# Optimization experiments

Hardware: AMD Instinct MI355X
Metric: run time of the kernel (lower is better)

Reference implementation:

```python
import jax, jax.numpy as jnp
import numpy as np

D_BRICK = 512  # args.brick_vector_dimension
H = 512        # hidden width


def setup_inputs() -> dict:
    key = jax.random.key(0)
    ks = jax.random.split(key, 20)
    B, N = 4, 192

    def w(k, shape, fan_in):
        return jax.random.uniform(k, shape, jnp.float32, -1.0, 1.0) / np.sqrt(fan_in)

    return {
        "brick_vectors": jax.random.normal(ks[0], (B, N, D_BRICK), jnp.float32),
        "xy": jax.random.uniform(ks[1], (B, N, 2), jnp.float32),
        # linear_xy: 2 -> 512
        "W_xy": w(ks[2], (H, 2), 2), "b_xy": w(ks[3], (H,), 2),
        # linear_a: D -> 512
        "W_a": w(ks[4], (H, D_BRICK), D_BRICK), "b_a": w(ks[5], (H,), D_BRICK),
        # linear_b: 512 -> 512
        "W_b": w(ks[6], (H, H), H), "b_b": w(ks[7], (H,), H),
        # combination_a: 1024 -> 512
        "W_ca": w(ks[8], (H, 2 * H), 2 * H), "b_ca": w(ks[9], (H,), 2 * H),
        # combination_b: 512 -> 512
        "W_cb": w(ks[10], (H, H), H), "b_cb": w(ks[11], (H,), H),
        # combination_c: 512 -> 512
        "W_cc": w(ks[12], (H, H), H), "b_cc": w(ks[13], (H,), H),
        # edge_out: 512 -> 2
        "W_out": w(ks[14], (2, H), H), "b_out": w(ks[15], (2,), H),
    }


def reference(brick_vectors, xy, W_xy, b_xy, W_a, b_a, W_b, b_b,
              W_ca, b_ca, W_cb, b_cb, W_cc, b_cc, W_out, b_out):
    # per-brick feature MLP: (B, N, 512)
    f = jnp.einsum('bnd,hd->bnh', brick_vectors, W_a) + b_a \
        + jnp.einsum('bnt,ht->bnh', xy, W_xy) + b_xy
    f = jax.nn.relu(f)
    f = jax.nn.relu(jnp.einsum('bnh,gh->bng', f, W_b) + b_b)

    # combination_a on concat(f[b,j], f[b,i]) without materializing the
    # (B, N, N, 1024) tensor: split the weight into the two 512 halves.
    # edge[b,i,j] = cat(features_a, features_b) where features_a = f[b,j]
    # (expanded over dim 1) and features_b = f[b,i] (expanded over dim 2).
    W1, W2 = W_ca[:, :H], W_ca[:, H:]
    u = jnp.einsum('bnh,gh->bng', f, W1)  # contribution from f[b, j]
    v = jnp.einsum('bnh,gh->bng', f, W2)  # contribution from f[b, i]
    e = jax.nn.relu(u[:, None, :, :] + v[:, :, None, :] + b_ca)  # (B,N,N,512)

    e = jax.nn.relu(jnp.einsum('bijh,gh->bijg', e, W_cb) + b_cb)
    e = jax.nn.relu(jnp.einsum('bijh,gh->bijg', e, W_cc) + b_cc)
    return jnp.einsum('bijh,oh->bijo', e, W_out) + b_out  # (B, N, N, 2)
```

## Files before the change

kernel.cpp:

```cpp
#include <hip/hip_runtime.h>


typedef short  short8  __attribute__((ext_vector_type(8)));
typedef short  short4v __attribute__((ext_vector_type(4)));
typedef float  f32x4   __attribute__((ext_vector_type(4)));

#define LDSW 520

__device__ inline unsigned short f2bf(float x) {
  unsigned u = __float_as_uint(x);
  unsigned r = (u + 0x7FFFu + ((u >> 16) & 1u)) >> 16;
  return (unsigned short)r;
}

__device__ __host__ inline int wtile_off(int c, int k) {
  return ((c >> 4) * 16 + (k >> 5)) * 512 + (c & 15) * 32 + (k & 31);
}

template <int MT, int NT>
__device__ inline void zero_acc(f32x4 (&acc)[MT][NT]) {
#pragma unroll
  for (int mt = 0; mt < MT; ++mt)
#pragma unroll
    for (int nt = 0; nt < NT; ++nt) {
      f32x4 z = {0.f, 0.f, 0.f, 0.f};
      acc[mt][nt] = z;
    }
}

template <int MT, int NT>
__device__ inline void gemm_kloop(const short* E, const short* __restrict__ W,
                                  int lane, int nbase, f32x4 (&acc)[MT][NT]) {
  const int mrow = lane & 15, kg = lane >> 4;
  const short* El = E + mrow * LDSW + kg * 8;
  const short* Wl = W + (nbase >> 4) * 8192 + mrow * 32 + kg * 8;
  short8 wF[2][NT];
#pragma unroll
  for (int nt = 0; nt < NT; ++nt) wF[0][nt] = *(const short8*)(Wl + nt * 8192);
#pragma unroll
  for (int ks = 0; ks < 16; ++ks) {
    const int cur = ks & 1, nxt = cur ^ 1;
    if (ks < 15) {
      const int k1 = (ks + 1) * 512;
#pragma unroll
      for (int nt = 0; nt < NT; ++nt)
        wF[nxt][nt] = *(const short8*)(Wl + nt * 8192 + k1);
    }
    const int k0 = ks * 32;
    short8 e0 = *(const short8*)(El + k0);
#pragma unroll
    for (int mt = 0; mt < MT; ++mt) {
      const short8 ecur = e0;
      if (mt < MT - 1) e0 = *(const short8*)(El + (mt + 1) * 16 * LDSW + k0);
#pragma unroll
      for (int nt = 0; nt < NT; ++nt)
        acc[mt][nt] = __builtin_amdgcn_mfma_f32_16x16x32_bf16(
            wF[cur][nt], ecur, acc[mt][nt], 0, 0, 0);
    }
  }
}

template <int MT, int NT>
__device__ inline void store_relu_lds(short* E, const float* __restrict__ bias,
                                      int lane, int nbase, f32x4 (&acc)[MT][NT]) {
  const int mrow = lane & 15, kg = lane >> 4;
#pragma unroll
  for (int nt = 0; nt < NT; ++nt) {
    const int oc = nbase + nt * 16 + kg * 4;
    const float4 bs = *(const float4*)(bias + oc);
#pragma unroll
    for (int mt = 0; mt < MT; ++mt) {
      short4v s;
      s.x = (short)f2bf(fmaxf(acc[mt][nt][0] + bs.x, 0.f));
      s.y = (short)f2bf(fmaxf(acc[mt][nt][1] + bs.y, 0.f));
      s.z = (short)f2bf(fmaxf(acc[mt][nt][2] + bs.z, 0.f));
      s.w = (short)f2bf(fmaxf(acc[mt][nt][3] + bs.w, 0.f));
      *(short4v*)&E[(mt * 16 + mrow) * LDSW + oc] = s;
    }
  }
}

__global__ void prep_kernel(const float* __restrict__ Wa, const float* __restrict__ Wb,
                            const float* __restrict__ Wca, const float* __restrict__ Wcb,
                            const float* __restrict__ Wcc, const float* __restrict__ Wout,
                            short* __restrict__ outS) {
  const int tid = blockIdx.x * blockDim.x + threadIdx.x;
  const int stride = gridDim.x * blockDim.x;
  const int M = 262144;
  for (int i = tid; i < 6 * M + 1024; i += stride) {
    float x;
    int dst;
    if (i < M) {
      const int c = i >> 9, k = i & 511;
      x = Wa[i];
      dst = wtile_off(c, k);
    } else if (i < 2 * M) {
      const int t = i - M, c = t >> 9, k = t & 511;
      x = Wb[t];
      dst = M + wtile_off(c, k);
    } else if (i < 3 * M) {
      const int t = i - 2 * M, c = t >> 9, k = t & 511;
      x = Wca[c * 1024 + k];
      dst = 2 * M + wtile_off(c, k);
    } else if (i < 4 * M) {
      const int t = i - 3 * M, c = t >> 9, k = t & 511;
      x = Wca[c * 1024 + 512 + k];
      dst = 2 * M + wtile_off(512 + c, k);
    } else if (i < 5 * M) {
      const int t = i - 4 * M, c = t >> 9, k = t & 511;
      x = Wcb[t];
      dst = 4 * M + wtile_off(c, k);
    } else if (i < 6 * M) {
      const int t = i - 5 * M, c = t >> 9, k = t & 511;
      x = Wcc[t];
      dst = 5 * M + wtile_off(c, k);
    } else {
      x = Wout[i - 6 * M];
      dst = i;
    }
    outS[dst] = (short)f2bf(x);
  }
}

template <int MODE>
__global__ __launch_bounds__(256, 4) void node_layer(
    const void* __restrict__ Xin, const short* __restrict__ W,
    const float* __restrict__ bias, const float* __restrict__ xy,
    const float* __restrict__ Wxy, const float* __restrict__ bxy,
    void* __restrict__ Yout, float* __restrict__ vout, int colTiles) {
  __shared__ short X[64 * LDSW];
  __shared__ float xyl[128];
  const int tid = threadIdx.x, lane = tid & 63, wave = tid >> 6;
  const int rt = blockIdx.x / colTiles, ct = blockIdx.x % colTiles;
  const int row0 = rt * 64, c0 = ct * 64;

  if (MODE == 1) {
    const float* bv = (const float*)Xin;
    const int hc = (tid & 127) * 4, m0 = tid >> 7;
    for (int m = m0; m < 64; m += 2) {
      const float4 t = *(const float4*)(bv + (row0 + m) * 512 + hc);
      short4v s;
      s.x = (short)f2bf(t.x); s.y = (short)f2bf(t.y);
      s.z = (short)f2bf(t.z); s.w = (short)f2bf(t.w);
      *(short4v*)&X[m * LDSW + hc] = s;
    }
    if (tid < 128) xyl[tid] = xy[row0 * 2 + tid];
  } else {
    const short* xb = (const short*)Xin;
    const int hc = (tid & 63) * 8, m0 = tid >> 6;
    for (int m = m0; m < 64; m += 4)
      *(short8*)&X[m * LDSW + hc] = *(const short8*)(xb + (row0 + m) * 512 + hc);
  }
  __syncthreads();

  const int nbase = c0 + wave * 16;
  f32x4 acc[4][1];
  zero_acc<4, 1>(acc);
  gemm_kloop<4, 1>(X, W, lane, nbase, acc);

  const int mrow = lane & 15, kg = lane >> 4;
  const int oc = nbase + kg * 4;
  if (MODE == 3) {
    float* u = (float*)Yout;
#pragma unroll
    for (int mt = 0; mt < 4; ++mt) {
      const int row = row0 + mt * 16 + mrow;
      if (oc < 512) *(f32x4*)&u[row * 512 + oc] = acc[mt][0];
      else          *(f32x4*)&vout[row * 512 + oc - 512] = acc[mt][0];
    }
  } else {
    short* Y = (short*)Yout;
    const float4 bs = *(const float4*)(bias + oc);
    float b2[4] = {0.f, 0.f, 0.f, 0.f}, w0[4], w1[4];
    if (MODE == 1) {
      const float4 t = *(const float4*)(bxy + oc);
      b2[0] = t.x; b2[1] = t.y; b2[2] = t.z; b2[3] = t.w;
#pragma unroll
      for (int r = 0; r < 4; ++r) { w0[r] = Wxy[(oc + r) * 2]; w1[r] = Wxy[(oc + r) * 2 + 1]; }
    }
#pragma unroll
    for (int mt = 0; mt < 4; ++mt) {
      const int row = mt * 16 + mrow;
      short4v s;
#pragma unroll
      for (int r = 0; r < 4; ++r) {
        float xv = acc[mt][0][r] + ((const float*)&bs)[r];
        if (MODE == 1) xv += b2[r] + xyl[row * 2] * w0[r] + xyl[row * 2 + 1] * w1[r];
        ((short*)&s)[r] = (short)f2bf(fmaxf(xv, 0.f));
      }
      *(short4v*)&Y[(row0 + row) * 512 + oc] = s;
    }
  }
}

__global__ __launch_bounds__(512, 2) void edge_kernel(
    const float* __restrict__ u, const float* __restrict__ v,
    const short* __restrict__ Wcb, const short* __restrict__ Wcc,
    const short* __restrict__ Wout,
    const float* __restrict__ bca, const float* __restrict__ bcb,
    const float* __restrict__ bcc, const float* __restrict__ bout,
    float* __restrict__ out) {
  __shared__ short A[144 * LDSW];
  __shared__ float red[144 * 2 * 8];
  const int tid = threadIdx.x, lane = tid & 63, wave = tid >> 6;
  const int blk = blockIdx.x;
  const int b = blk >> 8, rem = blk & 255, ip = rem >> 2, jt = rem & 3;
  const float* urow0 = u + (b * 192 + jt * 48) * 512;
  const float* vrow0 = v + (b * 192 + ip * 3) * 512;

  {
    const int hc = (tid & 127) * 4, m0 = tid >> 7;
    const float4 v0 = *(const float4*)(vrow0 + hc);
    const float4 v1 = *(const float4*)(vrow0 + 512 + hc);
    const float4 v2 = *(const float4*)(vrow0 + 1024 + hc);
    const float4 bb = *(const float4*)(bca + hc);
#pragma unroll 4
    for (int m = m0; m < 144; m += 4) {
      const int ii = (m >= 96) ? 2 : (m >= 48 ? 1 : 0);
      const int jj = m - ii * 48;
      const float4 vv = (ii == 0) ? v0 : (ii == 1) ? v1 : v2;
      const float4 uu = *(const float4*)(urow0 + jj * 512 + hc);
      short4v s;
      s.x = (short)f2bf(fmaxf(uu.x + vv.x + bb.x, 0.f));
      s.y = (short)f2bf(fmaxf(uu.y + vv.y + bb.y, 0.f));
      s.z = (short)f2bf(fmaxf(uu.z + vv.z + bb.z, 0.f));
      s.w = (short)f2bf(fmaxf(uu.w + vv.w + bb.w, 0.f));
      *(short4v*)&A[m * LDSW + hc] = s;
    }
  }
  __syncthreads();

  const int nbase = wave * 64;
  f32x4 acc[9][4];

  zero_acc<9, 4>(acc);
  gemm_kloop<9, 4>(A, Wcb, lane, nbase, acc);
  __syncthreads();
  store_relu_lds<9, 4>(A, bcb, lane, nbase, acc);
  __syncthreads();

  zero_acc<9, 4>(acc);
  gemm_kloop<9, 4>(A, Wcc, lane, nbase, acc);
  __syncthreads();
  store_relu_lds<9, 4>(A, bcc, lane, nbase, acc);
  __syncthreads();

  f32x4 oacc[9];
#pragma unroll
  for (int mt = 0; mt < 9; ++mt) { f32x4 z = {0.f, 0.f, 0.f, 0.f}; oacc[mt] = z; }
  const int n = lane & 15, kg2 = lane >> 4;
#pragma unroll
  for (int kk = 0; kk < 2; ++kk) {
    const int k0 = wave * 64 + kk * 32 + kg2 * 8;
    short8 bf = {0, 0, 0, 0, 0, 0, 0, 0};
    if (n < 2) bf = *(const short8*)(Wout + n * 512 + k0);
#pragma unroll
    for (int mt = 0; mt < 9; ++mt) {
      const short8 af = *(const short8*)(A + (mt * 16 + n) * LDSW + k0);
      oacc[mt] = __builtin_amdgcn_mfma_f32_16x16x32_bf16(af, bf, oacc[mt], 0, 0, 0);
    }
  }
  if (n < 2) {
#pragma unroll
    for (int mt = 0; mt < 9; ++mt)
#pragma unroll
      for (int r = 0; r < 4; ++r) {
        const int row = mt * 16 + kg2 * 4 + r;
        red[(row * 2 + n) * 8 + wave] = oacc[mt][r];
      }
  }
  __syncthreads();
  if (tid < 288) {
    const int row = tid >> 1, o = tid & 1;
    float s = bout[o];
#pragma unroll
    for (int w = 0; w < 8; ++w) s += red[(row * 2 + o) * 8 + w];
    const int ii = (row >= 96) ? 2 : (row >= 48 ? 1 : 0);
    const int jj = row - ii * 48;
    out[((b * 192 + ip * 3 + ii) * 192 + jt * 48 + jj) * 2 + o] = s;
  }
}

extern "C" void kernel_launch(void* const* d_in, const int* in_sizes, int n_in,
                              void* d_out, int out_size, void* d_ws, size_t ws_size,
                              hipStream_t stream) {
  const float* bv   = (const float*)d_in[0];
  const float* xy   = (const float*)d_in[1];
  const float* Wxy  = (const float*)d_in[2];
  const float* bxy  = (const float*)d_in[3];
  const float* Wa   = (const float*)d_in[4];
  const float* ba   = (const float*)d_in[5];
  const float* Wb   = (const float*)d_in[6];
  const float* bb   = (const float*)d_in[7];
  const float* Wca  = (const float*)d_in[8];
  const float* bca  = (const float*)d_in[9];
  const float* Wcb  = (const float*)d_in[10];
  const float* bcb  = (const float*)d_in[11];
  const float* Wcc  = (const float*)d_in[12];
  const float* bcc  = (const float*)d_in[13];
  const float* Wout = (const float*)d_in[14];
  const float* bout = (const float*)d_in[15];
  float* out = (float*)d_out;

  short* S = (short*)d_ws;
  char* base = (char*)d_ws;
  short* WaB   = S;
  short* WbB   = S + 262144;
  short* WuvB  = S + 524288;
  short* WcbB  = S + 1048576;
  short* WccB  = S + 1310720;
  short* WoutB = S + 1572864;
  short* f1 = (short*)(base + 3147776);
  float* u  = (float*)(base + 3147776);
  short* f2 = (short*)(base + 4720640);
  float* v  = (float*)(base + 5507072);

  prep_kernel<<<512, 256, 0, stream>>>(Wa, Wb, Wca, Wcb, Wcc, Wout, S);
  node_layer<1><<<96, 256, 0, stream>>>(bv, WaB, ba, xy, Wxy, bxy, f1, nullptr, 8);
  node_layer<2><<<96, 256, 0, stream>>>(f1, WbB, bb, nullptr, nullptr, nullptr, f2, nullptr, 8);
  node_layer<3><<<192, 256, 0, stream>>>(f2, WuvB, nullptr, nullptr, nullptr, nullptr, u, v, 16);
  edge_kernel<<<1024, 512, 0, stream>>>(u, v, WcbB, WccB, WoutB, bca, bcb, bcc, bout, out);
}
```

Measured before the change: 259.1 us.

## Retile edge kernel to 128-row blocks with 2x4 wave grid and XOR-swizzled LDS

The edge kernel now processes 128 edge rows per block (2 i by 64 j) instead of 144. Its 8 waves form a 2x4 grid, each computing a 64x128 output tile rather than a 144x64 strip, which changes how weight fragments and activations are reused per wave. LDS padding (row stride 520) is replaced by an XOR swizzle on 8-element chunks in all kernels, which removes bank conflicts without the padded footprint. Each wave now holds 32 accumulator tiles, which raises register pressure, and the grid grows from 1024 to 1152 blocks.

```diff
diff --git a/kernel.cpp b/kernel.cpp
--- a/kernel.cpp
+++ b/kernel.cpp
@@ -4,8 +4,6 @@
 typedef short  short8  __attribute__((ext_vector_type(8)));
 typedef short  short4v __attribute__((ext_vector_type(4)));
 typedef float  f32x4   __attribute__((ext_vector_type(4)));
-
-#define LDSW 520
 
 __device__ inline unsigned short f2bf(float x) {
   unsigned u = __float_as_uint(x);
@@ -13,6 +11,10 @@
   return (unsigned short)r;
 }
 
+__device__ inline int lds_e(int row, int e) {
+  return row * 512 + ((((e >> 3) ^ (row & 7)) << 3) | (e & 7));
+}
+
 __device__ __host__ inline int wtile_off(int c, int k) {
   return ((c >> 4) * 16 + (k >> 5)) * 512 + (c & 15) * 32 + (k & 31);
 }
@@ -31,8 +33,8 @@
 template <int MT, int NT>
 __device__ inline void gemm_kloop(const short* E, const short* __restrict__ W,
                                   int lane, int nbase, f32x4 (&acc)[MT][NT]) {
-  const int mrow = lane & 15, kg = lane >> 4;
-  const short* El = E + mrow * LDSW + kg * 8;
+  const int mrow = lane & 15, kg = lane >> 4, xorv = mrow & 7;
+  const short* El = E + mrow * 512;
   const short* Wl = W + (nbase >> 4) * 8192 + mrow * 32 + kg * 8;
   short8 wF[2][NT];
 #pragma unroll
@@ -46,12 +48,12 @@
       for (int nt = 0; nt < NT; ++nt)
         wF[nxt][nt] = *(const short8*)(Wl + nt * 8192 + k1);
     }
-    const int k0 = ks * 32;
-    short8 e0 = *(const short8*)(El + k0);
+    const int ch = ((ks * 4 + kg) ^ xorv) << 3;
+    short8 e0 = *(const short8*)(El + ch);
 #pragma unroll
     for (int mt = 0; mt < MT; ++mt) {
       const short8 ecur = e0;
-      if (mt < MT - 1) e0 = *(const short8*)(El + (mt + 1) * 16 * LDSW + k0);
+      if (mt < MT - 1) e0 = *(const short8*)(El + (mt + 1) * 8192 + ch);
 #pragma unroll
       for (int nt = 0; nt < NT; ++nt)
         acc[mt][nt] = __builtin_amdgcn_mfma_f32_16x16x32_bf16(
@@ -70,12 +72,13 @@
     const float4 bs = *(const float4*)(bias + oc);
 #pragma unroll
     for (int mt = 0; mt < MT; ++mt) {
+      const int row = mt * 16 + mrow;
       short4v s;
       s.x = (short)f2bf(fmaxf(acc[mt][nt][0] + bs.x, 0.f));
       s.y = (short)f2bf(fmaxf(acc[mt][nt][1] + bs.y, 0.f));
       s.z = (short)f2bf(fmaxf(acc[mt][nt][2] + bs.z, 0.f));
       s.w = (short)f2bf(fmaxf(acc[mt][nt][3] + bs.w, 0.f));
-      *(short4v*)&E[(mt * 16 + mrow) * LDSW + oc] = s;
+      *(short4v*)&E[lds_e(row, oc)] = s;
     }
   }
 }
@@ -128,7 +131,7 @@
     const float* __restrict__ bias, const float* __restrict__ xy,
     const float* __restrict__ Wxy, const float* __restrict__ bxy,
     void* __restrict__ Yout, float* __restrict__ vout, int colTiles) {
-  __shared__ short X[64 * LDSW];
+  __shared__ short X[64 * 512];
   __shared__ float xyl[128];
   const int tid = threadIdx.x, lane = tid & 63, wave = tid >> 6;
   const int rt = blockIdx.x / colTiles, ct = blockIdx.x % colTiles;
@@ -142,14 +145,14 @@
       short4v s;
       s.x = (short)f2bf(t.x); s.y = (short)f2bf(t.y);
       s.z = (short)f2bf(t.z); s.w = (short)f2bf(t.w);
-      *(short4v*)&X[m * LDSW + hc] = s;
+      *(short4v*)&X[lds_e(m, hc)] = s;
     }
     if (tid < 128) xyl[tid] = xy[row0 * 2 + tid];
   } else {
     const short* xb = (const short*)Xin;
     const int hc = (tid & 63) * 8, m0 = tid >> 6;
     for (int m = m0; m < 64; m += 4)
-      *(short8*)&X[m * LDSW + hc] = *(const short8*)(xb + (row0 + m) * 512 + hc);
+      *(short8*)&X[lds_e(m, hc)] = *(const short8*)(xb + (row0 + m) * 512 + hc);
   }
   __syncthreads();
 
@@ -200,84 +203,82 @@
     const float* __restrict__ bca, const float* __restrict__ bcb,
     const float* __restrict__ bcc, const float* __restrict__ bout,
     float* __restrict__ out) {
-  __shared__ short A[144 * LDSW];
-  __shared__ float red[144 * 2 * 8];
+  __shared__ short A[128 * 512];
+  __shared__ float red[128 * 2 * 8];
   const int tid = threadIdx.x, lane = tid & 63, wave = tid >> 6;
   const int blk = blockIdx.x;
-  const int b = blk >> 8, rem = blk & 255, ip = rem >> 2, jt = rem & 3;
-  const float* urow0 = u + (b * 192 + jt * 48) * 512;
-  const float* vrow0 = v + (b * 192 + ip * 3) * 512;
+  const int b = blk / 288, rem = blk % 288, ip = rem / 3, jt = rem % 3;
+  const float* urow0 = u + (b * 192 + jt * 64) * 512;
+  const float* vrow0 = v + (b * 192 + ip * 2) * 512;
 
   {
-    const int hc = (tid & 127) * 4, m0 = tid >> 7;
+    const int t = tid & 127, hc = t * 4, m0 = tid >> 7;
     const float4 v0 = *(const float4*)(vrow0 + hc);
     const float4 v1 = *(const float4*)(vrow0 + 512 + hc);
-    const float4 v2 = *(const float4*)(vrow0 + 1024 + hc);
     const float4 bb = *(const float4*)(bca + hc);
 #pragma unroll 4
-    for (int m = m0; m < 144; m += 4) {
-      const int ii = (m >= 96) ? 2 : (m >= 48 ? 1 : 0);
-      const int jj = m - ii * 48;
-      const float4 vv = (ii == 0) ? v0 : (ii == 1) ? v1 : v2;
-      const float4 uu = *(const float4*)(urow0 + jj * 512 + hc);
+    for (int m = m0; m < 128; m += 4) {
+      const float4 vv = (m >> 6) ? v1 : v0;
+      const float4 uu = *(const float4*)(urow0 + (m & 63) * 512 + hc);
       short4v s;
       s.x = (short)f2bf(fmaxf(uu.x + vv.x + bb.x, 0.f));
       s.y = (short)f2bf(fmaxf(uu.y + vv.y + bb.y, 0.f));
       s.z = (short)f2bf(fmaxf(uu.z + vv.z + bb.z, 0.f));
       s.w = (short)f2bf(fmaxf(uu.w + vv.w + bb.w, 0.f));
-      *(short4v*)&A[m * LDSW + hc] = s;
-    }
-  }
-  __syncthreads();
-
-  const int nbase = wave * 64;
-  f32x4 acc[9][4];
-
-  zero_acc<9, 4>(acc);
-  gemm_kloop<9, 4>(A, Wcb, lane, nbase, acc);
-  __syncthreads();
-  store_relu_lds<9, 4>(A, bcb, lane, nbase, acc);
-  __syncthreads();
-
-  zero_acc<9, 4>(acc);
-  gemm_kloop<9, 4>(A, Wcc, lane, nbase, acc);
-  __syncthreads();
-  store_relu_lds<9, 4>(A, bcc, lane, nbase, acc);
-  __syncthreads();
-
-  f32x4 oacc[9];
-#pragma unroll
-  for (int mt = 0; mt < 9; ++mt) { f32x4 z = {0.f, 0.f, 0.f, 0.f}; oacc[mt] = z; }
-  const int n = lane & 15, kg2 = lane >> 4;
+      *(short4v*)&A[lds_e(m, hc)] = s;
+    }
+  }
+  __syncthreads();
+
+  const int rg = wave >> 2, cg = wave & 3;
+  const int nbase = cg * 128;
+  short* Aw = A + (rg * 64) * 512;
+  f32x4 acc[4][8];
+
+  zero_acc<4, 8>(acc);
+  gemm_kloop<4, 8>(Aw, Wcb, lane, nbase, acc);
+  __syncthreads();
+  store_relu_lds<4, 8>(Aw, bcb, lane, nbase, acc);
+  __syncthreads();
+
+  zero_acc<4, 8>(acc);
+  gemm_kloop<4, 8>(Aw, Wcc, lane, nbase, acc);
+  __syncthreads();
+  store_relu_lds<4, 8>(Aw, bcc, lane, nbase, acc);
+  __syncthreads();
+
+  f32x4 oacc[8];
+#pragma unroll
+  for (int mt = 0; mt < 8; ++mt) { f32x4 z = {0.f, 0.f, 0.f, 0.f}; oacc[mt] = z; }
+  const int n2 = lane & 15, kg2 = lane >> 4;
 #pragma unroll
   for (int kk = 0; kk < 2; ++kk) {
-    const int k0 = wave * 64 + kk * 32 + kg2 * 8;
+    const int e = wave * 64 + kk * 32 + kg2 * 8;
     short8 bf = {0, 0, 0, 0, 0, 0, 0, 0};
-    if (n < 2) bf = *(const short8*)(Wout + n * 512 + k0);
-#pragma unroll
-    for (int mt = 0; mt < 9; ++mt) {
-      const short8 af = *(const short8*)(A + (mt * 16 + n) * LDSW + k0);
+    if (n2 < 2) bf = *(const short8*)(Wout + n2 * 512 + e);
+#pragma unroll
+    for (int mt = 0; mt < 8; ++mt) {
+      const short8 af = *(const short8*)&A[lds_e(mt * 16 + n2, e)];
       oacc[mt] = __builtin_amdgcn_mfma_f32_16x16x32_bf16(af, bf, oacc[mt], 0, 0, 0);
     }
   }
-  if (n < 2) {
-#pragma unroll
-    for (int mt = 0; mt < 9; ++mt)
+  if (n2 < 2) {
+#pragma unroll
+    for (int mt = 0; mt < 8; ++mt)
 #pragma unroll
       for (int r = 0; r < 4; ++r) {
         const int row = mt * 16 + kg2 * 4 + r;
-        red[(row * 2 + n) * 8 + wave] = oacc[mt][r];
+        red[(row * 2 + n2) * 8 + wave] = oacc[mt][r];
       }
   }
   __syncthreads();
-  if (tid < 288) {
+  if (tid < 256) {
     const int row = tid >> 1, o = tid & 1;
     float s = bout[o];
 #pragma unroll
     for (int w = 0; w < 8; ++w) s += red[(row * 2 + o) * 8 + w];
-    const int ii = (row >= 96) ? 2 : (row >= 48 ? 1 : 0);
-    const int jj = row - ii * 48;
-    out[((b * 192 + ip * 3 + ii) * 192 + jt * 48 + jj) * 2 + o] = s;
+    const int i = ip * 2 + (row >> 6), j = jt * 64 + (row & 63);
+    out[((b * 192 + i) * 192 + j) * 2 + o] = s;
   }
 }
 
@@ -319,5 +320,5 @@
   node_layer<1><<<96, 256, 0, stream>>>(bv, WaB, ba, xy, Wxy, bxy, f1, nullptr, 8);
   node_layer<2><<<96, 256, 0, stream>>>(f1, WbB, bb, nullptr, nullptr, nullptr, f2, nullptr, 8);
   node_layer<3><<<192, 256, 0, stream>>>(f2, WuvB, nullptr, nullptr, nullptr, nullptr, u, v, 16);
-  edge_kernel<<<1024, 512, 0, stream>>>(u, v, WcbB, WccB, WoutB, bca, bcb, bcc, bout, out);
-}
+  edge_kernel<<<1152, 512, 0, stream>>>(u, v, WcbB, WccB, WoutB, bca, bcb, bcc, bout, out);
+}
```

Measured after the change: 353.9 us. 1.37x slower.
